# Optimization experiments

Hardware: AMD Instinct MI355X
Metric: run time of the kernel (lower is better)

The kernel has to match this reference:

```python
import jax, jax.numpy as jnp
import numpy as np

FP8_MAX = 448.0  # max finite value of float8_e4m3fn
EPS = 1e-12


def _quantize_fp8(t):
    """Per-tensor dynamic fp8 quantization: returns (fp8_tensor, scale) where
    dequant = fp8.astype(f32) / scale, matching the torch module's math."""
    t32 = t.astype(jnp.float32)
    amax = jnp.maximum(jnp.max(jnp.abs(t32)), EPS)
    scale = FP8_MAX / amax
    t_fp8 = jnp.clip(t32 * scale, -FP8_MAX, FP8_MAX).astype(jnp.float8_e4m3fn)
    return t_fp8, scale


def setup_inputs() -> dict:
    key = jax.random.key(0)
    kx, kw, kb = jax.random.split(key, 3)
    M, K, N = 4096, 4096, 4096  # tokens, in_features, out_features
    x = jax.random.normal(kx, (M, K), dtype=jnp.float16)
    weight = jax.random.normal(kw, (N, K), dtype=jnp.float16)
    bias = jax.random.normal(kb, (N,), dtype=jnp.float16)
    return {"x": x, "weight": weight, "bias": bias}


def reference(x, weight, bias):
    # weight pre-quantization (quantize_weight)
    w_fp8, w_scale = _quantize_fp8(weight)
    # dynamic activation quantization
    x_fp8, x_scale = _quantize_fp8(x)
    # scaled_mm: (x_fp8 @ w_fp8.T) * scale_a * scale_b, out fp16
    acc = jnp.einsum(
        "mk,nk->mn",
        x_fp8.astype(jnp.float32),
        w_fp8.astype(jnp.float32),
        preferred_element_type=jnp.float32,
    )
    out = (acc * (1.0 / x_scale) * (1.0 / w_scale)).astype(jnp.float16)
    out = out + bias
    return out
```

## Files before the change

### kernel.cpp

```cpp
#include <hip/hip_runtime.h>
#include <hip/hip_fp16.h>

typedef __bf16 bf16x8 __attribute__((ext_vector_type(8)));
typedef float f32x4 __attribute__((ext_vector_type(4)));
typedef int i32x8 __attribute__((ext_vector_type(8)));
typedef unsigned short ushort8 __attribute__((ext_vector_type(8)));

#define BM 256
#define BN 256
#define BK 128
#define FP8MAX 448.0f
#define SCALE_ONE 0x7F7F7F7FU
#define A_BYTES (BM * BK)
#define B_BYTES (BN * BK)
#define SLOT_BYTES (A_BYTES + B_BYTES)

__global__ __launch_bounds__(256)
void amax_stage1(const float* __restrict__ x, unsigned n4x,
                 const float* __restrict__ w, unsigned n4w,
                 float* __restrict__ bm) {
    __shared__ float wmax[4];
    bool isw = blockIdx.x >= 1024;
    const float* in = isw ? w : x;
    unsigned n4 = isw ? n4w : n4x;
    unsigned tid = (blockIdx.x & 1023) * 256 + threadIdx.x;
    float m = 0.f;
    for (unsigned i = tid; i < n4; i += 1024 * 256) {
        float4 v = *(const float4*)(in + (size_t)i * 4);
        m = fmaxf(m, fmaxf(fmaxf(fabsf(v.x), fabsf(v.y)), fmaxf(fabsf(v.z), fabsf(v.w))));
    }
#pragma unroll
    for (int off = 32; off > 0; off >>= 1)
        m = fmaxf(m, __shfl_down(m, off));
    if ((threadIdx.x & 63) == 0) wmax[threadIdx.x >> 6] = m;
    __syncthreads();
    if (threadIdx.x == 0)
        bm[blockIdx.x] = fmaxf(fmaxf(wmax[0], wmax[1]), fmaxf(wmax[2], wmax[3]));
}

__global__ __launch_bounds__(256)
void amax_stage2(const float* __restrict__ bm, float* __restrict__ outv) {
    __shared__ float wmax[4];
    const float* p = bm + (size_t)blockIdx.x * 1024;
    float m = 0.f;
    for (int i = threadIdx.x; i < 1024; i += 256) m = fmaxf(m, p[i]);
#pragma unroll
    for (int off = 32; off > 0; off >>= 1)
        m = fmaxf(m, __shfl_down(m, off));
    if ((threadIdx.x & 63) == 0) wmax[threadIdx.x >> 6] = m;
    __syncthreads();
    if (threadIdx.x == 0)
        outv[blockIdx.x] = fmaxf(fmaxf(wmax[0], wmax[1]), fmaxf(wmax[2], wmax[3]));
}

__global__ __launch_bounds__(256)
void quant_kernel(const float* __restrict__ x, unsigned n8x,
                  const float* __restrict__ w, unsigned n8w,
                  unsigned char* __restrict__ xq, unsigned char* __restrict__ wq,
                  const float* __restrict__ amax2) {
    bool isw = blockIdx.x >= 2048;
    const float* in = isw ? w : x;
    uint2* out = (uint2*)(isw ? wq : xq);
    unsigned n8 = isw ? n8w : n8x;
    float amax = fmaxf(amax2[isw ? 1 : 0], 1e-12f);
    float scale = FP8MAX / amax;
    unsigned tid = (blockIdx.x & 2047) * 256 + threadIdx.x;
    for (unsigned i = tid; i < n8; i += 2048 * 256) {
        float4 lo = *(const float4*)(in + (size_t)i * 8);
        float4 hi = *(const float4*)(in + (size_t)i * 8 + 4);
        float f[8] = {lo.x, lo.y, lo.z, lo.w, hi.x, hi.y, hi.z, hi.w};
#pragma unroll
        for (int j = 0; j < 8; ++j)
            f[j] = fminf(fmaxf(f[j] * scale, -FP8MAX), FP8MAX);
        unsigned w0 = __builtin_amdgcn_cvt_pk_fp8_f32(f[0], f[1], 0u, false);
        w0 = __builtin_amdgcn_cvt_pk_fp8_f32(f[2], f[3], w0, true);
        unsigned w1 = __builtin_amdgcn_cvt_pk_fp8_f32(f[4], f[5], 0u, false);
        w1 = __builtin_amdgcn_cvt_pk_fp8_f32(f[6], f[7], w1, true);
        out[i] = make_uint2(w0, w1);
    }
}

__device__ inline void gl2lds16(const void* g, void* l) {
    __builtin_amdgcn_global_load_lds(
        (const __attribute__((address_space(1))) unsigned int*)g,
        (__attribute__((address_space(3))) unsigned int*)l, 16, 0, 0);
}

__global__ __launch_bounds__(512, 2)
void gemm_kernel(const unsigned char* __restrict__ A,
                 const unsigned char* __restrict__ B,
                 const float* __restrict__ bias,
                 float* __restrict__ C,
                 const float* __restrict__ amax2,
                 int M, int N, int K) {
    extern __shared__ char LDS[];

    int tid = threadIdx.x;
    int lane = tid & 63;
    int wave = tid >> 6;
    int wr = wave >> 2;
    int wcl = wave & 3;

    int nwg = gridDim.x;
    int nbx = N / BN;
    int q = nwg >> 3, r = nwg & 7;
    int xcd = blockIdx.x & 7, pos = blockIdx.x >> 3;
    int swz = (xcd < r ? xcd * (q + 1) : r * (q + 1) + (xcd - r) * q) + pos;
    int row0 = (swz / nbx) * BM;
    int col0 = (swz % nbx) * BN;

    f32x4 acc[8][4];
#pragma unroll
    for (int m = 0; m < 8; ++m)
#pragma unroll
        for (int n = 0; n < 4; ++n)
            acc[m][n] = (f32x4){0.f, 0.f, 0.f, 0.f};

    int frow = lane & 15;
    int g32 = (lane >> 4) * 32;

    const int NT = K >> 7;

    auto STAGE = [&](int t, int si) {
        char* slot = LDS + si * SLOT_BYTES;
#pragma unroll
        for (int i = 0; i < 4; ++i) {
            int s = i * 512 + tid;
            int rr = s >> 3, c = s & 7;
            gl2lds16(A + (size_t)(row0 + rr) * K + t * BK + ((c ^ (rr & 7)) << 4),
                     slot + s * 16);
        }
#pragma unroll
        for (int i = 0; i < 4; ++i) {
            int s = i * 512 + tid;
            int rr = s >> 3, c = s & 7;
            gl2lds16(B + (size_t)(col0 + rr) * K + t * BK + ((c ^ (rr & 7)) << 4),
                     slot + A_BYTES + s * 16);
        }
    };

    union U { i32x8 v; uint4 q[2]; };
    auto LDF = [&](U& u, const char* base, int row) {
        int c0 = g32 ^ ((row & 7) << 4);
        const char* p = base + row * 128;
        u.q[0] = *(const uint4*)(p + c0);
        u.q[1] = *(const uint4*)(p + (c0 ^ 16));
    };

    STAGE(0, 0);
    __syncthreads();

    int cur = 0;
    for (int t = 0; t < NT; ++t) {
        if (t + 1 < NT) STAGE(t + 1, cur ^ 1);

        const char* As = LDS + cur * SLOT_BYTES;
        const char* Bs = As + A_BYTES;

        U bf[4];
#pragma unroll
        for (int n = 0; n < 4; ++n)
            LDF(bf[n], Bs, wcl * 64 + n * 16 + frow);

        U af[8];
        LDF(af[0], As, wr * 128 + frow);
        LDF(af[1], As, wr * 128 + 16 + frow);

        __builtin_amdgcn_s_setprio(1);
#pragma unroll
        for (int m = 0; m < 8; ++m) {
            if (m + 2 < 8)
                LDF(af[m + 2], As, wr * 128 + (m + 2) * 16 + frow);
#pragma unroll
            for (int n = 0; n < 4; ++n)
                acc[m][n] = __builtin_amdgcn_mfma_scale_f32_16x16x128_f8f6f4(
                    af[m].v, bf[n].v, acc[m][n],
                    0, 0, 0, SCALE_ONE, 0, SCALE_ONE);
        }
        __builtin_amdgcn_s_setprio(0);

        __syncthreads();
        cur ^= 1;
    }

    float ax = fmaxf(amax2[0], 1e-12f);
    float aw = fmaxf(amax2[1], 1e-12f);
    float rs = (ax / FP8MAX) * (aw / FP8MAX);

    int crow0 = row0 + wr * 128;
    int ccol0 = col0 + wcl * 64 + frow;
    int rsub = (lane >> 4) * 4;
#pragma unroll
    for (int n = 0; n < 4; ++n) {
        int col = ccol0 + n * 16;
        float bv = bias[col];
#pragma unroll
        for (int m = 0; m < 8; ++m) {
#pragma unroll
            for (int j = 0; j < 4; ++j) {
                int row = crow0 + m * 16 + rsub + j;
                float tcl = __half2float(__float2half_rn(acc[m][n][j] * rs));
                C[(size_t)row * N + col] = __half2float(__float2half_rn(tcl + bv));
            }
        }
    }
}

__device__ inline ushort8 quant8f_bf16(float4 lo, float4 hi, float scale) {
    float f[8] = {lo.x, lo.y, lo.z, lo.w, hi.x, hi.y, hi.z, hi.w};
    ushort8 r;
#pragma unroll
    for (int j = 0; j < 4; ++j) {
        float f0 = fminf(fmaxf(f[2 * j] * scale, -FP8MAX), FP8MAX);
        float f1 = fminf(fmaxf(f[2 * j + 1] * scale, -FP8MAX), FP8MAX);
        unsigned pk = __builtin_amdgcn_cvt_pk_fp8_f32(f0, f1, 0u, false);
        float d0 = __builtin_amdgcn_cvt_f32_fp8(pk, 0);
        float d1 = __builtin_amdgcn_cvt_f32_fp8(pk, 1);
        r[2 * j]     = (unsigned short)(__float_as_uint(d0) >> 16);
        r[2 * j + 1] = (unsigned short)(__float_as_uint(d1) >> 16);
    }
    return r;
}

__global__ __launch_bounds__(256)
void gemm_fused(const float* __restrict__ X, const float* __restrict__ W,
                const float* __restrict__ bias, float* __restrict__ C,
                const float* __restrict__ amax2, int M, int N, int K) {
    __shared__ ushort8 As8[128 * 64 / 8];
    __shared__ ushort8 Bs8[128 * 64 / 8];
    char* As = (char*)As8;
    char* Bs = (char*)Bs8;

    float ax = fmaxf(amax2[0], 1e-12f);
    float aw = fmaxf(amax2[1], 1e-12f);
    float sx = FP8MAX / ax, sw = FP8MAX / aw;

    int tid = threadIdx.x;
    int lane = tid & 63;
    int wave = tid >> 6;
    int row0 = blockIdx.y * 128;
    int col0 = blockIdx.x * 128;
    int wr = wave >> 1, wc = wave & 1;

    f32x4 acc[4][4];
#pragma unroll
    for (int m = 0; m < 4; ++m)
#pragma unroll
        for (int n = 0; n < 4; ++n)
            acc[m][n] = (f32x4){0.f, 0.f, 0.f, 0.f};

    int frow = lane & 15;
    int fksub = (lane >> 4) * 16;

    for (int kt = 0; kt < K; kt += 64) {
#pragma unroll
        for (int i = 0; i < 4; ++i) {
            int s = i * 256 + tid;
            int r = s >> 3, c = s & 7;
            const float* pa = X + (size_t)(row0 + r) * K + kt + c * 8;
            const float* pb = W + (size_t)(col0 + r) * K + kt + c * 8;
            float4 a0 = *(const float4*)pa, a1 = *(const float4*)(pa + 4);
            float4 b0 = *(const float4*)pb, b1 = *(const float4*)(pb + 4);
            *(ushort8*)(As + s * 16) = quant8f_bf16(a0, a1, sx);
            *(ushort8*)(Bs + s * 16) = quant8f_bf16(b0, b1, sw);
        }
        __syncthreads();

#pragma unroll
        for (int kk = 0; kk < 2; ++kk) {
            bf16x8 af[4], bfr[4];
#pragma unroll
            for (int m = 0; m < 4; ++m)
                af[m] = *(const bf16x8*)(As + (wr * 64 + m * 16 + frow) * 128 + kk * 64 + fksub);
#pragma unroll
            for (int n = 0; n < 4; ++n)
                bfr[n] = *(const bf16x8*)(Bs + (wc * 64 + n * 16 + frow) * 128 + kk * 64 + fksub);
#pragma unroll
            for (int m = 0; m < 4; ++m)
#pragma unroll
                for (int n = 0; n < 4; ++n)
                    acc[m][n] = __builtin_amdgcn_mfma_f32_16x16x32_bf16(af[m], bfr[n], acc[m][n], 0, 0, 0);
        }
        __syncthreads();
    }

    float rs = (ax / FP8MAX) * (aw / FP8MAX);
    int crow0 = row0 + wr * 64;
    int ccol0 = col0 + wc * 64 + frow;
    int rsub = (lane >> 4) * 4;
#pragma unroll
    for (int n = 0; n < 4; ++n) {
        int col = ccol0 + n * 16;
        float bv = bias[col];
#pragma unroll
        for (int m = 0; m < 4; ++m) {
#pragma unroll
            for (int j = 0; j < 4; ++j) {
                int row = crow0 + m * 16 + rsub + j;
                float t = __half2float(__float2half_rn(acc[m][n][j] * rs));
                C[(size_t)row * N + col] = __half2float(__float2half_rn(t + bv));
            }
        }
    }
}

extern "C" void kernel_launch(void* const* d_in, const int* in_sizes, int n_in,
                              void* d_out, int out_size, void* d_ws, size_t ws_size,
                              hipStream_t stream) {
    const float* x = (const float*)d_in[0];
    const float* w = (const float*)d_in[1];
    const float* bias = (const float*)d_in[2];
    float* out = (float*)d_out;

    int N = in_sizes[2];
    int K = in_sizes[1] / N;
    int M = in_sizes[0] / K;

    float* bm = (float*)d_ws;
    float* amax2 = bm + 2048;
    unsigned char* xq = (unsigned char*)d_ws + 16384;
    unsigned char* wq = xq + (size_t)M * K;

    unsigned n4x = (unsigned)((size_t)M * K / 4);
    unsigned n4w = (unsigned)((size_t)N * K / 4);

    amax_stage1<<<2048, 256, 0, stream>>>(x, n4x, w, n4w, bm);
    amax_stage2<<<2, 256, 0, stream>>>(bm, amax2);

    size_t needA = (size_t)M * K + (size_t)N * K + 16384;

    if (ws_size >= needA && (M % BM) == 0 && (N % BN) == 0 && (K % BK) == 0 && K / BK >= 2) {
        quant_kernel<<<4096, 256, 0, stream>>>(x, (unsigned)((size_t)M * K / 8),
                                               w, (unsigned)((size_t)N * K / 8),
                                               xq, wq, amax2);
        int nwg = (M / BM) * (N / BN);
        gemm_kernel<<<nwg, 512, 2 * SLOT_BYTES, stream>>>(xq, wq, bias, out, amax2, M, N, K);
    } else {
        dim3 grid(N / 128, M / 128);
        gemm_fused<<<grid, 256, 0, stream>>>(x, w, bias, out, amax2, M, N, K);
    }
}
```

Baseline: 130.3 us.

## Prefetch two K-tiles ahead with fine-grained vmcnt waits and phased barriers

Stages tiles 0 and 1 before the loop. Inside the loop, the global->LDS load for tile t+2 is issued into the current slot once all waves have finished reading it. The main loop is split into four phases of two A-fragment rows each, with explicit lgkmcnt waits and s_barriers, a style similar to the ping-pong scheduling seen in hipBLASLt. Replacing __syncthreads with s_waitcnt vmcnt(8) lets one tile's loads stay in flight while the next is consumed, aiming to hide global memory latency. The extra barriers per iteration add synchronisation overhead, and the hand-counted vmcnt values must match the number of outstanding loads exactly.

Measured after the change: 173.8 us. 1.33x slower.

```diff
diff --git a/kernel.cpp b/kernel.cpp
--- a/kernel.cpp
+++ b/kernel.cpp
@@ -148,38 +148,64 @@
     };
 
     STAGE(0, 0);
-    __syncthreads();
+    if (NT > 1) {
+        STAGE(1, 1);
+        __builtin_amdgcn_sched_barrier(0);
+        asm volatile("s_waitcnt vmcnt(8)" ::: "memory");
+    } else {
+        __builtin_amdgcn_sched_barrier(0);
+        asm volatile("s_waitcnt vmcnt(0)" ::: "memory");
+    }
+    __builtin_amdgcn_s_barrier();
+    __builtin_amdgcn_sched_barrier(0);
 
     int cur = 0;
     for (int t = 0; t < NT; ++t) {
-        if (t + 1 < NT) STAGE(t + 1, cur ^ 1);
-
         const char* As = LDS + cur * SLOT_BYTES;
         const char* Bs = As + A_BYTES;
-
         U bf[4];
-#pragma unroll
-        for (int n = 0; n < 4; ++n)
-            LDF(bf[n], Bs, wcl * 64 + n * 16 + frow);
-
-        U af[8];
-        LDF(af[0], As, wr * 128 + frow);
-        LDF(af[1], As, wr * 128 + 16 + frow);
-
-        __builtin_amdgcn_s_setprio(1);
-#pragma unroll
-        for (int m = 0; m < 8; ++m) {
-            if (m + 2 < 8)
-                LDF(af[m + 2], As, wr * 128 + (m + 2) * 16 + frow);
+
+#pragma unroll
+        for (int p = 0; p < 4; ++p) {
+            if (p == 0) {
+#pragma unroll
+                for (int n = 0; n < 4; ++n)
+                    LDF(bf[n], Bs, wcl * 64 + n * 16 + frow);
+            }
+            U a0, a1;
+            LDF(a0, As, wr * 128 + (2 * p) * 16 + frow);
+            LDF(a1, As, wr * 128 + (2 * p + 1) * 16 + frow);
+
+            asm volatile("s_waitcnt lgkmcnt(0)" ::: "memory");
+            __builtin_amdgcn_sched_barrier(0);
+            __builtin_amdgcn_s_barrier();
+
+            if (p == 3 && t + 2 < NT)
+                STAGE(t + 2, cur);
+
+            __builtin_amdgcn_s_setprio(1);
 #pragma unroll
             for (int n = 0; n < 4; ++n)
-                acc[m][n] = __builtin_amdgcn_mfma_scale_f32_16x16x128_f8f6f4(
-                    af[m].v, bf[n].v, acc[m][n],
-                    0, 0, 0, SCALE_ONE, 0, SCALE_ONE);
-        }
-        __builtin_amdgcn_s_setprio(0);
-
-        __syncthreads();
+                acc[2 * p][n] = __builtin_amdgcn_mfma_scale_f32_16x16x128_f8f6f4(
+                    a0.v, bf[n].v, acc[2 * p][n], 0, 0, 0, SCALE_ONE, 0, SCALE_ONE);
+#pragma unroll
+            for (int n = 0; n < 4; ++n)
+                acc[2 * p + 1][n] = __builtin_amdgcn_mfma_scale_f32_16x16x128_f8f6f4(
+                    a1.v, bf[n].v, acc[2 * p + 1][n], 0, 0, 0, SCALE_ONE, 0, SCALE_ONE);
+            __builtin_amdgcn_s_setprio(0);
+
+            if (p < 3) __builtin_amdgcn_s_barrier();
+        }
+
+        if (t + 1 < NT) {
+            __builtin_amdgcn_sched_barrier(0);
+            if (t + 2 < NT)
+                asm volatile("s_waitcnt vmcnt(8)" ::: "memory");
+            else
+                asm volatile("s_waitcnt vmcnt(0)" ::: "memory");
+            __builtin_amdgcn_s_barrier();
+            __builtin_amdgcn_sched_barrier(0);
+        }
         cur ^= 1;
     }
 
```

## Load B fragments directly from global into registers, stage only A in LDS

Applied to the files above, without the earlier changes.

The GEMM no longer stages the weight tile in LDS. Each wave loads its B fragments straight from global memory into registers every K-step, while A stays double-buffered in LDS, and explicit vmcnt waits and barriers replace __syncthreads. This halves LDS use and LDS read traffic and may allow higher occupancy. In exchange, B rows are fetched redundantly by waves that share the same columns, global loads are less coalesced, and B load latency is exposed with no prefetch ahead of use.

Measured after the change: 160.1 us, median of 3. 1.23x slower.

```diff
diff --git a/kernel.cpp b/kernel.cpp
--- a/kernel.cpp
+++ b/kernel.cpp
@@ -12,8 +12,6 @@
 #define FP8MAX 448.0f
 #define SCALE_ONE 0x7F7F7F7FU
 #define A_BYTES (BM * BK)
-#define B_BYTES (BN * BK)
-#define SLOT_BYTES (A_BYTES + B_BYTES)
 
 __global__ __launch_bounds__(256)
 void amax_stage1(const float* __restrict__ x, unsigned n4x,
@@ -121,8 +119,8 @@
 
     const int NT = K >> 7;
 
-    auto STAGE = [&](int t, int si) {
-        char* slot = LDS + si * SLOT_BYTES;
+    auto STAGE_A = [&](int t, int si) {
+        char* slot = LDS + si * A_BYTES;
 #pragma unroll
         for (int i = 0; i < 4; ++i) {
             int s = i * 512 + tid;
@@ -130,56 +128,66 @@
             gl2lds16(A + (size_t)(row0 + rr) * K + t * BK + ((c ^ (rr & 7)) << 4),
                      slot + s * 16);
         }
-#pragma unroll
-        for (int i = 0; i < 4; ++i) {
-            int s = i * 512 + tid;
-            int rr = s >> 3, c = s & 7;
-            gl2lds16(B + (size_t)(col0 + rr) * K + t * BK + ((c ^ (rr & 7)) << 4),
-                     slot + A_BYTES + s * 16);
-        }
     };
 
     union U { i32x8 v; uint4 q[2]; };
-    auto LDF = [&](U& u, const char* base, int row) {
+    auto LDA = [&](U& u, const char* base, int row) {
         int c0 = g32 ^ ((row & 7) << 4);
         const char* p = base + row * 128;
         u.q[0] = *(const uint4*)(p + c0);
         u.q[1] = *(const uint4*)(p + (c0 ^ 16));
     };
 
-    STAGE(0, 0);
-    __syncthreads();
+    const unsigned char* Bbase = B + (size_t)(col0 + wcl * 64 + frow) * K + g32;
+
+    STAGE_A(0, 0);
+    asm volatile("s_waitcnt vmcnt(0)" ::: "memory");
+    __builtin_amdgcn_s_barrier();
+    __builtin_amdgcn_sched_barrier(0);
 
     int cur = 0;
     for (int t = 0; t < NT; ++t) {
-        if (t + 1 < NT) STAGE(t + 1, cur ^ 1);
-
-        const char* As = LDS + cur * SLOT_BYTES;
-        const char* Bs = As + A_BYTES;
-
         U bf[4];
 #pragma unroll
-        for (int n = 0; n < 4; ++n)
-            LDF(bf[n], Bs, wcl * 64 + n * 16 + frow);
-
+        for (int n = 0; n < 4; ++n) {
+            const unsigned char* bp = Bbase + (size_t)(n * 16) * K + t * BK;
+            bf[n].q[0] = *(const uint4*)bp;
+            bf[n].q[1] = *(const uint4*)(bp + 16);
+        }
+        __builtin_amdgcn_sched_barrier(0);
+
+        if (t + 1 < NT) STAGE_A(t + 1, cur ^ 1);
+
+        const char* As = LDS + cur * A_BYTES;
         U af[8];
-        LDF(af[0], As, wr * 128 + frow);
-        LDF(af[1], As, wr * 128 + 16 + frow);
+        LDA(af[0], As, wr * 128 + frow);
+        LDA(af[1], As, wr * 128 + 16 + frow);
+
+        __builtin_amdgcn_sched_barrier(0);
+        if (t + 1 < NT)
+            asm volatile("s_waitcnt vmcnt(4)" ::: "memory");
+        else
+            asm volatile("s_waitcnt vmcnt(0)" ::: "memory");
+        __builtin_amdgcn_sched_barrier(0);
 
         __builtin_amdgcn_s_setprio(1);
 #pragma unroll
         for (int m = 0; m < 8; ++m) {
             if (m + 2 < 8)
-                LDF(af[m + 2], As, wr * 128 + (m + 2) * 16 + frow);
+                LDA(af[m + 2], As, wr * 128 + (m + 2) * 16 + frow);
 #pragma unroll
             for (int n = 0; n < 4; ++n)
                 acc[m][n] = __builtin_amdgcn_mfma_scale_f32_16x16x128_f8f6f4(
-                    af[m].v, bf[n].v, acc[m][n],
-                    0, 0, 0, SCALE_ONE, 0, SCALE_ONE);
+                    af[m].v, bf[n].v, acc[m][n], 0, 0, 0, SCALE_ONE, 0, SCALE_ONE);
         }
         __builtin_amdgcn_s_setprio(0);
 
-        __syncthreads();
+        if (t + 1 < NT) {
+            __builtin_amdgcn_sched_barrier(0);
+            asm volatile("s_waitcnt vmcnt(0)" ::: "memory");
+            __builtin_amdgcn_s_barrier();
+            __builtin_amdgcn_sched_barrier(0);
+        }
         cur ^= 1;
     }
 
@@ -334,7 +342,7 @@
                                                w, (unsigned)((size_t)N * K / 8),
                                                xq, wq, amax2);
         int nwg = (M / BM) * (N / BN);
-        gemm_kernel<<<nwg, 512, 2 * SLOT_BYTES, stream>>>(xq, wq, bias, out, amax2, M, N, K);
+        gemm_kernel<<<nwg, 512, 2 * A_BYTES, stream>>>(xq, wq, bias, out, amax2, M, N, K);
     } else {
         dim3 grid(N / 128, M / 128);
         gemm_fused<<<grid, 256, 0, stream>>>(x, w, bias, out, amax2, M, N, K);
```

## Split MFMA main loop into barrier-synchronized phases with explicit LDS prefetch

Applied to the files above, without the earlier changes.

Replaces the unrolled A-fragment loop with four explicit phases. Each phase starts with a workgroup barrier, an lgkmcnt wait and a scheduling barrier, then issues MFMAs interleaved with prefetches of the next A fragments. The aim is to keep waves in lockstep so LDS reads and MFMA bursts line up across waves, with the compiler prevented from reordering across phases. It adds three extra barriers per K-tile, which may stall waves and cut the overlap between LDS loads and MFMAs.

Result: slower. 133.5 us (+2.4%).

```diff
diff --git a/kernel.cpp b/kernel.cpp
--- a/kernel.cpp
+++ b/kernel.cpp
@@ -140,13 +140,28 @@
     };
 
     union U { i32x8 v; uint4 q[2]; };
-    auto LDF = [&](U& u, const char* base, int row) {
+    auto LDA = [&](U& u, const char* base, int row) {
         int c0 = g32 ^ ((row & 7) << 4);
         const char* p = base + row * 128;
         u.q[0] = *(const uint4*)(p + c0);
         u.q[1] = *(const uint4*)(p + (c0 ^ 16));
     };
 
+#define MFMA4(am, AV)                                                              \
+    do {                                                                           \
+        _Pragma("unroll")                                                          \
+        for (int n = 0; n < 4; ++n)                                                \
+            acc[am][n] = __builtin_amdgcn_mfma_scale_f32_16x16x128_f8f6f4(         \
+                (AV).v, bf[n].v, acc[am][n], 0, 0, 0, SCALE_ONE, 0, SCALE_ONE);    \
+    } while (0)
+
+#define PHASE_SYNC()                                          \
+    do {                                                      \
+        __builtin_amdgcn_s_barrier();                         \
+        asm volatile("s_waitcnt lgkmcnt(0)" ::: "memory");    \
+        __builtin_amdgcn_sched_barrier(0);                    \
+    } while (0)
+
     STAGE(0, 0);
     __syncthreads();
 
@@ -156,32 +171,51 @@
 
         const char* As = LDS + cur * SLOT_BYTES;
         const char* Bs = As + A_BYTES;
+        int arow = wr * 128 + frow;
 
         U bf[4];
 #pragma unroll
         for (int n = 0; n < 4; ++n)
-            LDF(bf[n], Bs, wcl * 64 + n * 16 + frow);
-
-        U af[8];
-        LDF(af[0], As, wr * 128 + frow);
-        LDF(af[1], As, wr * 128 + 16 + frow);
-
+            LDA(bf[n], Bs, wcl * 64 + n * 16 + frow);
+        U a0, a1, a2, a3, a4, a5, a6, a7;
+        LDA(a0, As, arow);
+        LDA(a1, As, arow + 16);
+
+        PHASE_SYNC();
         __builtin_amdgcn_s_setprio(1);
-#pragma unroll
-        for (int m = 0; m < 8; ++m) {
-            if (m + 2 < 8)
-                LDF(af[m + 2], As, wr * 128 + (m + 2) * 16 + frow);
-#pragma unroll
-            for (int n = 0; n < 4; ++n)
-                acc[m][n] = __builtin_amdgcn_mfma_scale_f32_16x16x128_f8f6f4(
-                    af[m].v, bf[n].v, acc[m][n],
-                    0, 0, 0, SCALE_ONE, 0, SCALE_ONE);
-        }
+        MFMA4(0, a0);
+        LDA(a2, As, arow + 32);
+        LDA(a3, As, arow + 48);
+        MFMA4(1, a1);
+        __builtin_amdgcn_s_setprio(0);
+
+        PHASE_SYNC();
+        __builtin_amdgcn_s_setprio(1);
+        MFMA4(2, a2);
+        LDA(a4, As, arow + 64);
+        LDA(a5, As, arow + 80);
+        MFMA4(3, a3);
+        __builtin_amdgcn_s_setprio(0);
+
+        PHASE_SYNC();
+        __builtin_amdgcn_s_setprio(1);
+        MFMA4(4, a4);
+        LDA(a6, As, arow + 96);
+        LDA(a7, As, arow + 112);
+        MFMA4(5, a5);
+        __builtin_amdgcn_s_setprio(0);
+
+        PHASE_SYNC();
+        __builtin_amdgcn_s_setprio(1);
+        MFMA4(6, a6);
+        MFMA4(7, a7);
         __builtin_amdgcn_s_setprio(0);
 
         __syncthreads();
         cur ^= 1;
     }
+#undef MFMA4
+#undef PHASE_SYNC
 
     float ax = fmaxf(amax2[0], 1e-12f);
     float aw = fmaxf(amax2[1], 1e-12f);
```
